# Kernel tuning notes

Hardware: AMD Instinct MI355X
Metric: run time of the kernel (lower is better)

Reference implementation:

```python
import jax, jax.numpy as jnp
import numpy as np

N = 4_000_000   # number of sparse voxels
H = 128         # parent-grid extent per axis (input coords < 256 -> parents < 128)


def setup_inputs() -> dict:
    key = jax.random.key(0)
    # col 0 = batch index, cols 1:4 = integer xyz voxel coords in [0, 256)
    coords = jax.random.randint(key, (N, 4), 0, 256, dtype=jnp.int32)
    # spnn.Conv3d(1,1,k=2) kernel: (2^3, in=1, out=1), constant-init to 1.0
    kernel = jnp.ones((8, 1, 1), dtype=jnp.float32)
    return {"coords": coords, "kernel": kernel}


def _fog(coords, kernel):
    b = coords[:, 0].astype(jnp.int64)
    xyz = coords[:, 1:]
    # pos(): 3-bit occupancy code from LSBs of xyz, feat = 2^code
    bits = xyz & 1                                        # (N, 3)
    pos = bits[:, 0] + 2 * bits[:, 1] + 4 * bits[:, 2]    # (N,) in [0, 8)
    feats = (jnp.int32(1) << pos).astype(jnp.float32)     # (N,) values {1,...,128}

    # 2x2x2 stride-2 sparse conv with all-ones kernel == sum over the 8 children
    # of each parent voxel. The child's kernel-offset index is exactly `pos`.
    pxyz = (xyz >> 1).astype(jnp.int64)                   # parent coords
    pkey = ((b * H + pxyz[:, 0]) * H + pxyz[:, 1]) * H + pxyz[:, 2]

    ukeys, inv = jnp.unique(pkey, size=N, fill_value=-1, return_inverse=True)
    inv = inv.ravel()

    contrib = feats * kernel[pos, 0, 0]                   # all-ones kernel -> feats
    out_feats = jax.ops.segment_sum(contrib, inv, num_segments=N)  # (N,)

    # decode unique parent keys back to (batch, x, y, z); pad slots -> -1
    valid = ukeys >= 0
    k = jnp.where(valid, ukeys, 0)
    oz = k % H
    k = k // H
    oy = k % H
    k = k // H
    ox = k % H
    ob = k // H
    out_coords = jnp.stack([ob, ox, oy, oz], axis=-1).astype(jnp.int32)
    out_coords = jnp.where(valid[:, None], out_coords, jnp.int32(-1))
    return out_coords, out_feats


def reference(coords, kernel):
    return _fog(coords, kernel)
```

## Files before the change

### kernel.cpp

```cpp
#include <hip/hip_runtime.h>

#define NB_BITS     11
#define N_BUCKETS   (1 << NB_BITS)
#define LOCAL_BITS  18
#define LOCAL_WORDS 8192
#define LKMASK      ((1u << LOCAL_BITS) - 1u)
#define KEYMASK     0x1FFFFFFFu
#define NXCD        8
#define WCAP        512
#define WSHIFT      9
#define FE_CAP      2560
#define PPT         8
#define TILE        (1024 * PPT)

#define ST_AGG      (1u << 30)
#define ST_PRE      (2u << 30)
#define VALMASK     0x3FFFFFFFu

__device__ __forceinline__ unsigned make_key(int4 c) {
    return ((((unsigned)c.x << 7) | (unsigned)(c.y >> 1)) << 7 | (unsigned)(c.z >> 1)) << 7
         | (unsigned)(c.w >> 1);
}

template<int NW>
__device__ inline void block_scan(unsigned v, unsigned* wsum, unsigned& excl, unsigned& total) {
    int t = threadIdx.x, ln = t & 63, wv = t >> 6;
    unsigned incl = v;
    #pragma unroll
    for (int off = 1; off < 64; off <<= 1) {
        unsigned y = __shfl_up(incl, off, 64);
        if (ln >= off) incl += y;
    }
    if (ln == 63) wsum[wv] = incl;
    __syncthreads();
    if (wv == 0) {
        unsigned s = (ln < NW) ? wsum[ln] : 0u;
        #pragma unroll
        for (int off = 1; off < NW; off <<= 1) {
            unsigned y = __shfl_up(s, off, 64);
            if (ln >= off) s += y;
        }
        if (ln < NW) wsum[ln] = s;
    }
    __syncthreads();
    excl = (wv ? wsum[wv - 1] : 0u) + incl - v;
    total = wsum[NW - 1];
}

__global__ void __launch_bounds__(1024, 4)
build_pass(const int4* __restrict__ coords,
           unsigned* __restrict__ gcur,
           unsigned* __restrict__ pairs,
           int n) {
    __shared__ unsigned h[N_BUCKETS];
    __shared__ unsigned sk[TILE];
    int t = threadIdx.x, blk = blockIdx.x;
    unsigned xcd = (unsigned)blk & 7u;
    int base = blk * TILE;
    h[t] = 0u; h[t + 1024] = 0u;
    __syncthreads();
    #pragma unroll
    for (int m = 0; m < PPT; ++m) {
        int i = base + t + m * 1024;
        if (i < n) {
            int4 c = coords[i];
            unsigned key = make_key(c);
            unsigned pos = (unsigned)((c.y & 1) | ((c.z & 1) << 1) | ((c.w & 1) << 2));
            unsigned s = (pos << 29) | key;
            sk[t + m * 1024] = s;
            atomicAdd(&h[key >> LOCAL_BITS], 1u);
        }
    }
    __syncthreads();
    #pragma unroll
    for (int q = 0; q < 2; ++q) {
        int j = t + q * 1024;
        unsigned c = h[j];
        if (c) h[j] = atomicAdd(&gcur[((unsigned)j << 3) | xcd], c);
        else   h[j] = 0u;
    }
    __syncthreads();
    #pragma unroll
    for (int m = 0; m < PPT; ++m) {
        int i = base + t + m * 1024;
        if (i < n) {
            unsigned s = sk[t + m * 1024];
            unsigned b = (s & KEYMASK) >> LOCAL_BITS;
            unsigned o = atomicAdd(&h[b], 1u);
            if (o < WCAP)
                pairs[(((b << 3) | xcd) << WSHIFT) + o] = s;
        }
    }
}

__global__ void __launch_bounds__(1024, 2)
emit_pass(const unsigned* __restrict__ pairs,
          const unsigned* __restrict__ gcur,
          unsigned* __restrict__ pub,
          const float* __restrict__ kern,
          float4* __restrict__ out_coords,
          float* __restrict__ out_feats, int n) {
    __shared__ unsigned       bm[LOCAL_WORDS];
    __shared__ unsigned short pfx[LOCAL_WORDS];
    __shared__ float          fe[FE_CAP];
    __shared__ unsigned wsum[16];
    __shared__ unsigned gb[NXCD + 1];
    __shared__ unsigned ubS;
    __shared__ float    kl[8];
    int t = threadIdx.x, b = blockIdx.x;
    if (t < 8) kl[t] = (float)(1 << t) * kern[t];
    ((uint4*)bm)[t] = make_uint4(0u, 0u, 0u, 0u);
    ((uint4*)bm)[t + 1024] = make_uint4(0u, 0u, 0u, 0u);
    for (int i = t; i < FE_CAP; i += 1024) fe[i] = 0.f;
    if (t == 0) {
        unsigned r = 0;
        #pragma unroll
        for (int g = 0; g < NXCD; ++g) {
            gb[g] = r;
            r += min(gcur[((unsigned)b << 3) | g], (unsigned)WCAP);
        }
        gb[NXCD] = r;
    }
    __syncthreads();
    unsigned tot = gb[NXCD];
    for (unsigned p = (unsigned)t; p < tot; p += 1024) {
        unsigned g = 0;
        #pragma unroll
        for (int k = 1; k < NXCD; ++k) g += (p >= gb[k]) ? 1u : 0u;
        unsigned lk = pairs[((((unsigned)b << 3) | g) << WSHIFT) + (p - gb[g])] & LKMASK;
        atomicOr(&bm[lk >> 5], 1u << (lk & 31u));
    }
    __syncthreads();
    uint4 q0 = ((uint4*)bm)[2 * t], q1 = ((uint4*)bm)[2 * t + 1];
    unsigned pc[8] = { (unsigned)__popc(q0.x), (unsigned)__popc(q0.y),
                       (unsigned)__popc(q0.z), (unsigned)__popc(q0.w),
                       (unsigned)__popc(q1.x), (unsigned)__popc(q1.y),
                       (unsigned)__popc(q1.z), (unsigned)__popc(q1.w) };
    unsigned psum = 0;
    #pragma unroll
    for (int m = 0; m < 8; ++m) psum += pc[m];
    unsigned excl, cnt;
    block_scan<16>(psum, wsum, excl, cnt);
    if (t == 0)
        __hip_atomic_store(&pub[b], ST_AGG | cnt, __ATOMIC_RELAXED, __HIP_MEMORY_SCOPE_AGENT);
    unsigned run = excl;
    #pragma unroll
    for (int m = 0; m < 8; ++m) { pfx[8 * t + m] = (unsigned short)run; run += pc[m]; }
    if (t < 64) {
        unsigned sum = 0;
        if (b > 0) {
            int j = b - 1;
            while (true) {
                int idx = j - 63 + t;
                unsigned v = (idx >= 0)
                    ? __hip_atomic_load(&pub[idx], __ATOMIC_RELAXED, __HIP_MEMORY_SCOPE_AGENT)
                    : (ST_PRE | 0u);
                unsigned st = v >> 30;
                unsigned long long vm = __ballot(st != 0u);
                if (vm != ~0ull) continue;
                unsigned long long pm = __ballot(st == 2u);
                unsigned val = v & VALMASK;
                if (pm) {
                    int lp = 63 - __clzll(pm);
                    unsigned red = (t >= lp) ? val : 0u;
                    #pragma unroll
                    for (int off = 1; off < 64; off <<= 1) red += __shfl_xor(red, off, 64);
                    sum += red;
                    break;
                }
                unsigned red = val;
                #pragma unroll
                for (int off = 1; off < 64; off <<= 1) red += __shfl_xor(red, off, 64);
                sum += red;
                j -= 64;
            }
        }
        if (t == 0) {
            __hip_atomic_store(&pub[b], ST_PRE | (sum + cnt),
                               __ATOMIC_RELAXED, __HIP_MEMORY_SCOPE_AGENT);
            ubS = sum;
        }
    }
    __syncthreads();
    unsigned ub = ubS;
    unsigned wq[8] = { q0.x, q0.y, q0.z, q0.w, q1.x, q1.y, q1.z, q1.w };
    unsigned r2 = excl;
    #pragma unroll
    for (int m = 0; m < 8; ++m) {
        unsigned w = wq[m];
        unsigned hi = ((unsigned)b << LOCAL_BITS) | ((unsigned)(8 * t + m) << 5);
        while (w) {
            unsigned bit = (unsigned)__ffs(w) - 1u;
            w &= w - 1u;
            unsigned key = hi | bit;
            out_coords[ub + r2] = make_float4((float)(key >> 21),
                                              (float)((key >> 14) & 127u),
                                              (float)((key >> 7) & 127u),
                                              (float)(key & 127u));
            ++r2;
        }
    }
    for (unsigned p = (unsigned)t; p < tot; p += 1024) {
        unsigned g = 0;
        #pragma unroll
        for (int k = 1; k < NXCD; ++k) g += (p >= gb[k]) ? 1u : 0u;
        unsigned pk = pairs[((((unsigned)b << 3) | g) << WSHIFT) + (p - gb[g])];
        unsigned lk = pk & LKMASK;
        unsigned wd = lk >> 5;
        unsigned lr = (unsigned)pfx[wd] + __popc(bm[wd] & ((1u << (lk & 31u)) - 1u));
        atomicAdd(&fe[lr], kl[pk >> 29]);
    }
    __syncthreads();
    for (unsigned i = (unsigned)t; i < cnt; i += 1024)
        out_feats[ub + i] = fe[i];
}

__global__ void tail_pass(const unsigned* __restrict__ pub,
                          float4* __restrict__ out_coords,
                          float* __restrict__ out_feats, int n) {
    unsigned T = pub[N_BUCKETS - 1] & VALMASK;
    unsigned gid = blockIdx.x * blockDim.x + threadIdx.x;
    unsigned stride = gridDim.x * blockDim.x;
    for (unsigned r = T + gid; r < (unsigned)n; r += stride) {
        out_coords[r] = make_float4(-1.f, -1.f, -1.f, -1.f);
        out_feats[r] = 0.f;
    }
}

extern "C" void kernel_launch(void* const* d_in, const int* in_sizes, int n_in,
                              void* d_out, int out_size, void* d_ws, size_t ws_size,
                              hipStream_t stream) {
    const int4* coords = (const int4*)d_in[0];
    const float* kern  = (const float*)d_in[1];
    int N = in_sizes[0] / 4;

    float* out = (float*)d_out;
    float4* out_coords = (float4*)out;
    float* out_feats = out + (size_t)4 * N;

    unsigned* pairs = (unsigned*)d_ws;
    unsigned* gcur  = pairs + (size_t)N_BUCKETS * NXCD * WCAP;
    unsigned* pub   = gcur + (size_t)N_BUCKETS * NXCD;

    hipMemsetAsync(gcur, 0, (size_t)(N_BUCKETS * NXCD + N_BUCKETS) * sizeof(unsigned), stream);

    int ntiles = (N + TILE - 1) / TILE;
    build_pass<<<ntiles, 1024, 0, stream>>>(coords, gcur, pairs, N);
    emit_pass<<<N_BUCKETS, 1024, 0, stream>>>(pairs, gcur, pub, kern, out_coords, out_feats, N);
    tail_pass<<<256, 256, 0, stream>>>(pub, out_coords, out_feats, N);
}
```

Before: 235.3 us.

## Overlap feature scatter with lookback and recompute keys instead of staging in LDS

In build_pass, the shared-memory key tile is dropped; coords are re-read and keys recomputed in the scatter pass, cutting LDS use so more blocks can be resident. In emit_pass, the per-XCD offset prefix is computed by a warp shuffle scan instead of a serial loop. The pairs are now cached in registers by waves 1-15, which run the feature accumulation while wave 0 performs the decoupled lookback. Both kernels raise the launch_bounds occupancy hint to 8, which tightens the register budget and risks spills, and build_pass now reads coords from global memory twice.

```diff
diff --git a/kernel.cpp b/kernel.cpp
--- a/kernel.cpp
+++ b/kernel.cpp
@@ -47,17 +47,32 @@
     total = wsum[NW - 1];
 }
 
-__global__ void __launch_bounds__(1024, 4)
+__global__ void __launch_bounds__(1024, 8)
 build_pass(const int4* __restrict__ coords,
            unsigned* __restrict__ gcur,
            unsigned* __restrict__ pairs,
            int n) {
     __shared__ unsigned h[N_BUCKETS];
-    __shared__ unsigned sk[TILE];
     int t = threadIdx.x, blk = blockIdx.x;
     unsigned xcd = (unsigned)blk & 7u;
     int base = blk * TILE;
     h[t] = 0u; h[t + 1024] = 0u;
+    __syncthreads();
+    #pragma unroll
+    for (int m = 0; m < PPT; ++m) {
+        int i = base + t + m * 1024;
+        if (i < n) {
+            int4 c = coords[i];
+            atomicAdd(&h[make_key(c) >> LOCAL_BITS], 1u);
+        }
+    }
+    __syncthreads();
+    #pragma unroll
+    for (int q = 0; q < 2; ++q) {
+        int j = t + q * 1024;
+        unsigned c = h[j];
+        h[j] = c ? atomicAdd(&gcur[((unsigned)j << 3) | xcd], c) : 0u;
+    }
     __syncthreads();
     #pragma unroll
     for (int m = 0; m < PPT; ++m) {
@@ -66,34 +81,15 @@
             int4 c = coords[i];
             unsigned key = make_key(c);
             unsigned pos = (unsigned)((c.y & 1) | ((c.z & 1) << 1) | ((c.w & 1) << 2));
-            unsigned s = (pos << 29) | key;
-            sk[t + m * 1024] = s;
-            atomicAdd(&h[key >> LOCAL_BITS], 1u);
-        }
-    }
-    __syncthreads();
-    #pragma unroll
-    for (int q = 0; q < 2; ++q) {
-        int j = t + q * 1024;
-        unsigned c = h[j];
-        if (c) h[j] = atomicAdd(&gcur[((unsigned)j << 3) | xcd], c);
-        else   h[j] = 0u;
-    }
-    __syncthreads();
-    #pragma unroll
-    for (int m = 0; m < PPT; ++m) {
-        int i = base + t + m * 1024;
-        if (i < n) {
-            unsigned s = sk[t + m * 1024];
-            unsigned b = (s & KEYMASK) >> LOCAL_BITS;
+            unsigned b = key >> LOCAL_BITS;
             unsigned o = atomicAdd(&h[b], 1u);
             if (o < WCAP)
-                pairs[(((b << 3) | xcd) << WSHIFT) + o] = s;
-        }
-    }
-}
-
-__global__ void __launch_bounds__(1024, 2)
+                pairs[(((b << 3) | xcd) << WSHIFT) + o] = (pos << 29) | key;
+        }
+    }
+}
+
+__global__ void __launch_bounds__(1024, 8)
 emit_pass(const unsigned* __restrict__ pairs,
           const unsigned* __restrict__ gcur,
           unsigned* __restrict__ pub,
@@ -108,27 +104,41 @@
     __shared__ unsigned ubS;
     __shared__ float    kl[8];
     int t = threadIdx.x, b = blockIdx.x;
-    if (t < 8) kl[t] = (float)(1 << t) * kern[t];
+    unsigned gv = 0;
+    if (t < 8) {
+        kl[t] = (float)(1 << t) * kern[t];
+        gv = min(gcur[((unsigned)b << 3) | t], (unsigned)WCAP);
+    }
+    if (t < 64) {
+        unsigned incl = gv;
+        #pragma unroll
+        for (int off = 1; off < 8; off <<= 1) {
+            unsigned y = __shfl_up(incl, off, 64);
+            if (t >= off) incl += y;
+        }
+        if (t < 8) gb[t + 1] = incl;
+        if (t == 0) gb[0] = 0u;
+    }
     ((uint4*)bm)[t] = make_uint4(0u, 0u, 0u, 0u);
     ((uint4*)bm)[t + 1024] = make_uint4(0u, 0u, 0u, 0u);
     for (int i = t; i < FE_CAP; i += 1024) fe[i] = 0.f;
-    if (t == 0) {
-        unsigned r = 0;
-        #pragma unroll
-        for (int g = 0; g < NXCD; ++g) {
-            gb[g] = r;
-            r += min(gcur[((unsigned)b << 3) | g], (unsigned)WCAP);
-        }
-        gb[NXCD] = r;
-    }
     __syncthreads();
     unsigned tot = gb[NXCD];
-    for (unsigned p = (unsigned)t; p < tot; p += 1024) {
-        unsigned g = 0;
-        #pragma unroll
-        for (int k = 1; k < NXCD; ++k) g += (p >= gb[k]) ? 1u : 0u;
-        unsigned lk = pairs[((((unsigned)b << 3) | g) << WSHIFT) + (p - gb[g])] & LKMASK;
-        atomicOr(&bm[lk >> 5], 1u << (lk & 31u));
+    unsigned pk[5];
+    if (t >= 64) {
+        #pragma unroll
+        for (int k = 0; k < 5; ++k) {
+            unsigned p = (unsigned)(t - 64) + (unsigned)k * 960u;
+            if (p < tot) {
+                unsigned g = 0;
+                #pragma unroll
+                for (int j = 1; j < NXCD; ++j) g += (p >= gb[j]) ? 1u : 0u;
+                unsigned v = pairs[((((unsigned)b << 3) | g) << WSHIFT) + (p - gb[g])];
+                pk[k] = v;
+                unsigned lk = v & LKMASK;
+                atomicOr(&bm[lk >> 5], 1u << (lk & 31u));
+            }
+        }
     }
     __syncthreads();
     uint4 q0 = ((uint4*)bm)[2 * t], q1 = ((uint4*)bm)[2 * t + 1];
@@ -146,7 +156,20 @@
     unsigned run = excl;
     #pragma unroll
     for (int m = 0; m < 8; ++m) { pfx[8 * t + m] = (unsigned short)run; run += pc[m]; }
-    if (t < 64) {
+    __syncthreads();
+    if (t >= 64) {
+        #pragma unroll
+        for (int k = 0; k < 5; ++k) {
+            unsigned p = (unsigned)(t - 64) + (unsigned)k * 960u;
+            if (p < tot) {
+                unsigned v = pk[k];
+                unsigned lk = v & LKMASK;
+                unsigned wd = lk >> 5;
+                unsigned lr = (unsigned)pfx[wd] + __popc(bm[wd] & ((1u << (lk & 31u)) - 1u));
+                atomicAdd(&fe[lr], kl[v >> 29]);
+            }
+        }
+    } else {
         unsigned sum = 0;
         if (b > 0) {
             int j = b - 1;
@@ -200,17 +223,6 @@
             ++r2;
         }
     }
-    for (unsigned p = (unsigned)t; p < tot; p += 1024) {
-        unsigned g = 0;
-        #pragma unroll
-        for (int k = 1; k < NXCD; ++k) g += (p >= gb[k]) ? 1u : 0u;
-        unsigned pk = pairs[((((unsigned)b << 3) | g) << WSHIFT) + (p - gb[g])];
-        unsigned lk = pk & LKMASK;
-        unsigned wd = lk >> 5;
-        unsigned lr = (unsigned)pfx[wd] + __popc(bm[wd] & ((1u << (lk & 31u)) - 1u));
-        atomicAdd(&fe[lr], kl[pk >> 29]);
-    }
-    __syncthreads();
     for (unsigned i = (unsigned)t; i < cnt; i += 1024)
         out_feats[ub + i] = fe[i];
 }
```

Result: slower. 243.3 us (+3.4%).

## Replace bucketed pair scatter with global occupancy bitmap, scan, and atomic feature pass

Applied to the files above, without the earlier changes.

Drops the two-level bucketing (per-block histograms, pairs buffer, per-bucket local bitmaps) and instead marks every parent key in a global 2^29-bit bitmap with global atomicOr. A decoupled-lookback scan over the bitmap writes the compacted coordinates plus coarse prefix counts. A third pass re-reads the coordinates, computes each voxel's rank from the coarse prefix and popcounts, and atomically adds its feature into the output. This removes the WCAP overflow cap and pair traffic, but needs a 64 MB bitmap memset and full bitmap read, scattered global atomics, and a second read of the coordinates.

```diff
diff --git a/kernel.cpp b/kernel.cpp
--- a/kernel.cpp
+++ b/kernel.cpp
@@ -1,17 +1,10 @@
 #include <hip/hip_runtime.h>
 
-#define NB_BITS     11
-#define N_BUCKETS   (1 << NB_BITS)
-#define LOCAL_BITS  18
-#define LOCAL_WORDS 8192
-#define LKMASK      ((1u << LOCAL_BITS) - 1u)
-#define KEYMASK     0x1FFFFFFFu
-#define NXCD        8
-#define WCAP        512
-#define WSHIFT      9
-#define FE_CAP      2560
-#define PPT         8
-#define TILE        (1024 * PPT)
+#define KEY_BITS    29
+#define BM_WORDS    (1u << (KEY_BITS - 5))
+#define NLINES      (1u << (KEY_BITS - 9))
+#define NCOARSE     (1u << (KEY_BITS - 7))
+#define SCAN_BLOCKS (NLINES / 1024)
 
 #define ST_AGG      (1u << 30)
 #define ST_PRE      (2u << 30)
@@ -47,105 +40,42 @@
     total = wsum[NW - 1];
 }
 
-__global__ void __launch_bounds__(1024, 4)
-build_pass(const int4* __restrict__ coords,
-           unsigned* __restrict__ gcur,
-           unsigned* __restrict__ pairs,
-           int n) {
-    __shared__ unsigned h[N_BUCKETS];
-    __shared__ unsigned sk[TILE];
-    int t = threadIdx.x, blk = blockIdx.x;
-    unsigned xcd = (unsigned)blk & 7u;
-    int base = blk * TILE;
-    h[t] = 0u; h[t + 1024] = 0u;
-    __syncthreads();
-    #pragma unroll
-    for (int m = 0; m < PPT; ++m) {
-        int i = base + t + m * 1024;
-        if (i < n) {
-            int4 c = coords[i];
-            unsigned key = make_key(c);
-            unsigned pos = (unsigned)((c.y & 1) | ((c.z & 1) << 1) | ((c.w & 1) << 2));
-            unsigned s = (pos << 29) | key;
-            sk[t + m * 1024] = s;
-            atomicAdd(&h[key >> LOCAL_BITS], 1u);
-        }
+__global__ void __launch_bounds__(256)
+mark_pass(const int4* __restrict__ coords,
+          unsigned* __restrict__ bm,
+          float4* __restrict__ feats4, int n) {
+    int gid = blockIdx.x * 256 + threadIdx.x;
+    int stride = gridDim.x * 256;
+    for (int i = gid; i < n; i += stride) {
+        int4 c = coords[i];
+        unsigned key = make_key(c);
+        atomicOr(&bm[key >> 5], 1u << (key & 31u));
     }
-    __syncthreads();
-    #pragma unroll
-    for (int q = 0; q < 2; ++q) {
-        int j = t + q * 1024;
-        unsigned c = h[j];
-        if (c) h[j] = atomicAdd(&gcur[((unsigned)j << 3) | xcd], c);
-        else   h[j] = 0u;
-    }
-    __syncthreads();
-    #pragma unroll
-    for (int m = 0; m < PPT; ++m) {
-        int i = base + t + m * 1024;
-        if (i < n) {
-            unsigned s = sk[t + m * 1024];
-            unsigned b = (s & KEYMASK) >> LOCAL_BITS;
-            unsigned o = atomicAdd(&h[b], 1u);
-            if (o < WCAP)
-                pairs[(((b << 3) | xcd) << WSHIFT) + o] = s;
-        }
-    }
+    int nq = n >> 2;
+    for (int i = gid; i < nq; i += stride)
+        feats4[i] = make_float4(0.f, 0.f, 0.f, 0.f);
 }
 
 __global__ void __launch_bounds__(1024, 2)
-emit_pass(const unsigned* __restrict__ pairs,
-          const unsigned* __restrict__ gcur,
+scan_pass(const uint4* __restrict__ bm4,
+          unsigned* __restrict__ coarse,
           unsigned* __restrict__ pub,
-          const float* __restrict__ kern,
-          float4* __restrict__ out_coords,
-          float* __restrict__ out_feats, int n) {
-    __shared__ unsigned       bm[LOCAL_WORDS];
-    __shared__ unsigned short pfx[LOCAL_WORDS];
-    __shared__ float          fe[FE_CAP];
+          float4* __restrict__ out_coords) {
     __shared__ unsigned wsum[16];
-    __shared__ unsigned gb[NXCD + 1];
-    __shared__ unsigned ubS;
-    __shared__ float    kl[8];
+    __shared__ unsigned baseS;
     int t = threadIdx.x, b = blockIdx.x;
-    if (t < 8) kl[t] = (float)(1 << t) * kern[t];
-    ((uint4*)bm)[t] = make_uint4(0u, 0u, 0u, 0u);
-    ((uint4*)bm)[t + 1024] = make_uint4(0u, 0u, 0u, 0u);
-    for (int i = t; i < FE_CAP; i += 1024) fe[i] = 0.f;
-    if (t == 0) {
-        unsigned r = 0;
-        #pragma unroll
-        for (int g = 0; g < NXCD; ++g) {
-            gb[g] = r;
-            r += min(gcur[((unsigned)b << 3) | g], (unsigned)WCAP);
-        }
-        gb[NXCD] = r;
-    }
-    __syncthreads();
-    unsigned tot = gb[NXCD];
-    for (unsigned p = (unsigned)t; p < tot; p += 1024) {
-        unsigned g = 0;
-        #pragma unroll
-        for (int k = 1; k < NXCD; ++k) g += (p >= gb[k]) ? 1u : 0u;
-        unsigned lk = pairs[((((unsigned)b << 3) | g) << WSHIFT) + (p - gb[g])] & LKMASK;
-        atomicOr(&bm[lk >> 5], 1u << (lk & 31u));
-    }
-    __syncthreads();
-    uint4 q0 = ((uint4*)bm)[2 * t], q1 = ((uint4*)bm)[2 * t + 1];
-    unsigned pc[8] = { (unsigned)__popc(q0.x), (unsigned)__popc(q0.y),
-                       (unsigned)__popc(q0.z), (unsigned)__popc(q0.w),
-                       (unsigned)__popc(q1.x), (unsigned)__popc(q1.y),
-                       (unsigned)__popc(q1.z), (unsigned)__popc(q1.w) };
-    unsigned psum = 0;
-    #pragma unroll
-    for (int m = 0; m < 8; ++m) psum += pc[m];
-    unsigned excl, cnt;
-    block_scan<16>(psum, wsum, excl, cnt);
+    unsigned L = (unsigned)b * 1024u + (unsigned)t;
+    uint4 W0 = bm4[4u * L + 0u], W1 = bm4[4u * L + 1u];
+    uint4 W2 = bm4[4u * L + 2u], W3 = bm4[4u * L + 3u];
+    unsigned pcg0 = __popc(W0.x) + __popc(W0.y) + __popc(W0.z) + __popc(W0.w);
+    unsigned pcg1 = __popc(W1.x) + __popc(W1.y) + __popc(W1.z) + __popc(W1.w);
+    unsigned pcg2 = __popc(W2.x) + __popc(W2.y) + __popc(W2.z) + __popc(W2.w);
+    unsigned pcg3 = __popc(W3.x) + __popc(W3.y) + __popc(W3.z) + __popc(W3.w);
+    unsigned psum = pcg0 + pcg1 + pcg2 + pcg3;
+    unsigned excl, tot;
+    block_scan<16>(psum, wsum, excl, tot);
     if (t == 0)
-        __hip_atomic_store(&pub[b], ST_AGG | cnt, __ATOMIC_RELAXED, __HIP_MEMORY_SCOPE_AGENT);
-    unsigned run = excl;
-    #pragma unroll
-    for (int m = 0; m < 8; ++m) { pfx[8 * t + m] = (unsigned short)run; run += pc[m]; }
+        __hip_atomic_store(&pub[b], ST_AGG | tot, __ATOMIC_RELAXED, __HIP_MEMORY_SCOPE_AGENT);
     if (t < 64) {
         unsigned sum = 0;
         if (b > 0) {
@@ -176,55 +106,63 @@
             }
         }
         if (t == 0) {
-            __hip_atomic_store(&pub[b], ST_PRE | (sum + cnt),
+            __hip_atomic_store(&pub[b], ST_PRE | (sum + tot),
                                __ATOMIC_RELAXED, __HIP_MEMORY_SCOPE_AGENT);
-            ubS = sum;
+            baseS = sum;
         }
     }
     __syncthreads();
-    unsigned ub = ubS;
-    unsigned wq[8] = { q0.x, q0.y, q0.z, q0.w, q1.x, q1.y, q1.z, q1.w };
-    unsigned r2 = excl;
+    unsigned rr = baseS + excl;
+    unsigned words[16] = { W0.x, W0.y, W0.z, W0.w, W1.x, W1.y, W1.z, W1.w,
+                           W2.x, W2.y, W2.z, W2.w, W3.x, W3.y, W3.z, W3.w };
     #pragma unroll
-    for (int m = 0; m < 8; ++m) {
-        unsigned w = wq[m];
-        unsigned hi = ((unsigned)b << LOCAL_BITS) | ((unsigned)(8 * t + m) << 5);
+    for (int k = 0; k < 16; ++k) {
+        if ((k & 3) == 0) coarse[4u * L + (unsigned)(k >> 2)] = rr;
+        unsigned w = words[k];
+        unsigned hi = (L << 9) | ((unsigned)k << 5);
         while (w) {
             unsigned bit = (unsigned)__ffs(w) - 1u;
             w &= w - 1u;
             unsigned key = hi | bit;
-            out_coords[ub + r2] = make_float4((float)(key >> 21),
-                                              (float)((key >> 14) & 127u),
-                                              (float)((key >> 7) & 127u),
-                                              (float)(key & 127u));
-            ++r2;
+            out_coords[rr++] = make_float4((float)(key >> 21),
+                                           (float)((key >> 14) & 127u),
+                                           (float)((key >> 7) & 127u),
+                                           (float)(key & 127u));
         }
     }
-    for (unsigned p = (unsigned)t; p < tot; p += 1024) {
-        unsigned g = 0;
-        #pragma unroll
-        for (int k = 1; k < NXCD; ++k) g += (p >= gb[k]) ? 1u : 0u;
-        unsigned pk = pairs[((((unsigned)b << 3) | g) << WSHIFT) + (p - gb[g])];
-        unsigned lk = pk & LKMASK;
-        unsigned wd = lk >> 5;
-        unsigned lr = (unsigned)pfx[wd] + __popc(bm[wd] & ((1u << (lk & 31u)) - 1u));
-        atomicAdd(&fe[lr], kl[pk >> 29]);
-    }
-    __syncthreads();
-    for (unsigned i = (unsigned)t; i < cnt; i += 1024)
-        out_feats[ub + i] = fe[i];
 }
 
-__global__ void tail_pass(const unsigned* __restrict__ pub,
-                          float4* __restrict__ out_coords,
-                          float* __restrict__ out_feats, int n) {
-    unsigned T = pub[N_BUCKETS - 1] & VALMASK;
-    unsigned gid = blockIdx.x * blockDim.x + threadIdx.x;
-    unsigned stride = gridDim.x * blockDim.x;
-    for (unsigned r = T + gid; r < (unsigned)n; r += stride) {
-        out_coords[r] = make_float4(-1.f, -1.f, -1.f, -1.f);
-        out_feats[r] = 0.f;
+__global__ void __launch_bounds__(256)
+feat_pass(const int4* __restrict__ coords,
+          const uint4* __restrict__ bm4,
+          const unsigned* __restrict__ coarse,
+          const unsigned* __restrict__ pub,
+          const float* __restrict__ kern,
+          float4* __restrict__ out_coords,
+          float* __restrict__ out_feats, int n) {
+    __shared__ float kl[8];
+    if (threadIdx.x < 8) kl[threadIdx.x] = (float)(1 << threadIdx.x) * kern[threadIdx.x];
+    __syncthreads();
+    int gid = blockIdx.x * 256 + threadIdx.x;
+    int stride = gridDim.x * 256;
+    for (int i = gid; i < n; i += stride) {
+        int4 c = coords[i];
+        unsigned key = make_key(c);
+        unsigned pos = (unsigned)((c.y & 1) | ((c.z & 1) << 1) | ((c.w & 1) << 2));
+        unsigned g = key >> 7;
+        uint4 W = bm4[g];
+        unsigned r = coarse[g];
+        unsigned w2 = (key >> 5) & 3u;
+        r += (w2 > 0) ? __popc(W.x) : 0u;
+        r += (w2 > 1) ? __popc(W.y) : 0u;
+        r += (w2 > 2) ? __popc(W.z) : 0u;
+        unsigned sel = (w2 == 0) ? W.x : (w2 == 1) ? W.y : (w2 == 2) ? W.z : W.w;
+        r += __popc(sel & ((1u << (key & 31u)) - 1u));
+        atomicAdd(&out_feats[r], kl[pos]);
     }
+    unsigned T = pub[SCAN_BLOCKS - 1] & VALMASK;
+    for (unsigned row = T + (unsigned)gid; row < (unsigned)n; row += (unsigned)stride)
+        out_coords[row] = make_float4(-1.f, -1.f, -1.f, -1.f);
 }
 
 extern "C" void kernel_launch(void* const* d_in, const int* in_sizes, int n_in,
@@ -238,14 +176,14 @@
     float4* out_coords = (float4*)out;
     float* out_feats = out + (size_t)4 * N;
 
-    unsigned* pairs = (unsigned*)d_ws;
-    unsigned* gcur  = pairs + (size_t)N_BUCKETS * NXCD * WCAP;
-    unsigned* pub   = gcur + (size_t)N_BUCKETS * NXCD;
+    unsigned* bm     = (unsigned*)d_ws;
+    unsigned* pub    = bm + (size_t)BM_WORDS;
+    unsigned* coarse = pub + (size_t)SCAN_BLOCKS;
 
-    hipMemsetAsync(gcur, 0, (size_t)(N_BUCKETS * NXCD + N_BUCKETS) * sizeof(unsigned), stream);
+    hipMemsetAsync(bm, 0, ((size_t)BM_WORDS + SCAN_BLOCKS) * sizeof(unsigned), stream);
 
-    int ntiles = (N + TILE - 1) / TILE;
-    build_pass<<<ntiles, 1024, 0, stream>>>(coords, gcur, pairs, N);
-    emit_pass<<<N_BUCKETS, 1024, 0, stream>>>(pairs, gcur, pub, kern, out_coords, out_feats, N);
-    tail_pass<<<256, 256, 0, stream>>>(pub, out_coords, out_feats, N);
+    mark_pass<<<2048, 256, 0, stream>>>(coords, bm, (float4*)out_feats, N);
+    scan_pass<<<SCAN_BLOCKS, 1024, 0, stream>>>((const uint4*)bm, coarse, pub, out_coords);
+    feat_pass<<<2048, 256, 0, stream>>>(coords, (const uint4*)bm, coarse, pub, kern,
+                                        out_coords, out_feats, N);
 }
```

New measurement: 538.1 us. 129% more time.
